# Kernel optimization log

Hardware: AMD Instinct MI355X
Metric: run time of the kernel (lower is better)

Reference implementation:

```python
import jax, jax.numpy as jnp
import numpy as np

NUM_LOCAL = 4      # num_local_experts
E_TOTAL = 8        # local + unpopular experts
HIDDEN = 1024
FFN = 4 * HIDDEN
CAP = 2048         # tokens (capacity) per expert
D0 = 1             # leading dim of inputs / output_tensor


def setup_inputs() -> dict:
    key = jax.random.key(0)
    k_in, k_w0, k_w3 = jax.random.split(key, 3)
    inputs = jax.random.normal(k_in, (D0, E_TOTAL, CAP, HIDDEN), dtype=jnp.float32)
    # gating-activity indicator per expert; all-ones -> all unpopular experts active
    output_tensor = jnp.ones((D0, E_TOTAL), dtype=jnp.float32)
    # stacked per-expert MLP weights (torch Linear convention: [out, in])
    w0 = jax.random.normal(k_w0, (E_TOTAL, FFN, HIDDEN), dtype=jnp.float32) * 0.02
    w3 = jax.random.normal(k_w3, (E_TOTAL, HIDDEN, FFN), dtype=jnp.float32) * 0.02
    return {"output_tensor": output_tensor, "inputs": inputs, "w0": w0, "w3": w3}


def reference(output_tensor, inputs, w0, w3):
    # Grouped 2-layer MLP per expert: x @ w0^T -> GELU -> @ w3^T
    # b: D0, e: expert, c: capacity, d: hidden, f: ffn
    h = jnp.einsum('becd,efd->becf', inputs, w0)
    h = jax.nn.gelu(h, approximate=False)  # torch nn.GELU default = exact erf
    out = jnp.einsum('becf,edf->becd', h, w3)
    # unpopular experts with zero activity produce zeros (scatter-into-zeros combine)
    unpop_mask = jnp.sum(output_tensor[:, NUM_LOCAL:], axis=0) != 0  # [E_unpop]
    full_mask = jnp.concatenate(
        [jnp.ones((NUM_LOCAL,), dtype=bool), unpop_mask])  # locals always computed
    out = out * full_mask[None, :, None, None].astype(out.dtype)
    return out
```

## Files before the change

### kernel.cpp

```cpp
#include <hip/hip_runtime.h>
#include <math.h>

#define E_TOTAL 8
#define NUM_LOCAL 4
#define HIDDEN 1024
#define FFN 4096
#define CAP 2048

typedef unsigned short ushort_t;
typedef __attribute__((ext_vector_type(8))) short short8;
typedef __attribute__((ext_vector_type(8))) unsigned short u16x8;
typedef __attribute__((ext_vector_type(4))) float f32x4;

__device__ __forceinline__ unsigned short f2bf(float f) {
  unsigned int u = __float_as_uint(f);
  u += 0x7FFFu + ((u >> 16) & 1u);
  return (unsigned short)(u >> 16);
}

__device__ __forceinline__ void gload_lds16(const void* g, void* l) {
  __builtin_amdgcn_global_load_lds(
      (const __attribute__((address_space(1))) void*)g,
      (__attribute__((address_space(3))) void*)l,
      16, 0, 0);
}

__global__ __launch_bounds__(256) void cvt_kernel(const float4* __restrict__ s,
                                                  u16x8* __restrict__ d) {
  const size_t i = (size_t)blockIdx.x * 256 + threadIdx.x;
  float4 a = s[2 * i], b = s[2 * i + 1];
  u16x8 o;
  o[0] = f2bf(a.x); o[1] = f2bf(a.y); o[2] = f2bf(a.z); o[3] = f2bf(a.w);
  o[4] = f2bf(b.x); o[5] = f2bf(b.y); o[6] = f2bf(b.z); o[7] = f2bf(b.w);
  d[i] = o;
}

template <int M, int N, int K, bool GELU_OUT>
__global__ __launch_bounds__(256, 2) void gemm_nt(
    const ushort_t* __restrict__ A, const ushort_t* __restrict__ B,
    void* __restrict__ Cout, const float* __restrict__ ot, int d0) {
  __shared__ ushort_t lds_a[128 * 64];
  __shared__ ushort_t lds_b[128 * 64];

  const int e = blockIdx.z;
  const int bm = blockIdx.x * 128;
  const int bn = blockIdx.y * 128;
  const int t = threadIdx.x;
  const int wave = t >> 6, lane = t & 63;
  const int wr = wave >> 1, wc = wave & 1;
  const int quad = lane >> 4, l16 = lane & 15;
  const int r8 = lane >> 3;
  const int s8 = lane & 7;
  const int g8 = (s8 + r8) & 7;

  const ushort_t* Ag = A + (size_t)e * M * K + (size_t)(bm + r8) * K + g8 * 8;
  const ushort_t* Bg = B + (size_t)e * N * K + (size_t)(bn + r8) * K + g8 * 8;

  f32x4 acc[4][4];
#pragma unroll
  for (int i = 0; i < 4; ++i)
#pragma unroll
    for (int j = 0; j < 4; ++j) {
      f32x4 z = {0.f, 0.f, 0.f, 0.f};
      acc[i][j] = z;
    }

  for (int kb = 0; kb < K / 64; ++kb) {
    const size_t ko = (size_t)kb * 64;
#pragma unroll
    for (int j = 0; j < 4; ++j) {
      const int R = (j * 4 + wave) * 8;
      gload_lds16(Ag + ko + (size_t)R * K, &lds_a[R * 64]);
      gload_lds16(Bg + ko + (size_t)R * K, &lds_b[R * 64]);
    }
    __syncthreads();

#pragma unroll
    for (int ks = 0; ks < 2; ++ks) {
      short8 af[4], bfr[4];
      const int c = ks * 4 + quad;
#pragma unroll
      for (int i = 0; i < 4; ++i) {
        const int ra = wr * 64 + i * 16 + l16;
        const int rb = wc * 64 + i * 16 + l16;
        af[i]  = *(const short8*)&lds_a[ra * 64 + ((c - ra) & 7) * 8];
        bfr[i] = *(const short8*)&lds_b[rb * 64 + ((c - rb) & 7) * 8];
      }
#pragma unroll
      for (int mi = 0; mi < 4; ++mi)
#pragma unroll
        for (int ni = 0; ni < 4; ++ni)
          acc[mi][ni] = __builtin_amdgcn_mfma_f32_16x16x32_bf16(
              af[mi], bfr[ni], acc[mi][ni], 0, 0, 0);
    }
    __syncthreads();
  }

  if (GELU_OUT) {
    ushort_t* C = (ushort_t*)Cout + (size_t)e * M * N +
                  (size_t)(bm + wr * 64) * N + (bn + wc * 64);
#pragma unroll
    for (int mi = 0; mi < 4; ++mi)
#pragma unroll
      for (int r = 0; r < 4; ++r) {
        const int row = mi * 16 + quad * 4 + r;
#pragma unroll
        for (int ni = 0; ni < 4; ++ni) {
          float v = acc[mi][ni][r];
          v = 0.5f * v * (1.f + erff(v * 0.70710678118654752f));
          C[(size_t)row * N + ni * 16 + l16] = f2bf(v);
        }
      }
  } else {
    float mask = 1.f;
    if (e >= NUM_LOCAL) {
      float s = 0.f;
      for (int b = 0; b < d0; ++b) s += ot[b * E_TOTAL + e];
      mask = (s != 0.f) ? 1.f : 0.f;
    }
    float* C = (float*)Cout + (size_t)e * M * N +
               (size_t)(bm + wr * 64) * N + (bn + wc * 64);
#pragma unroll
    for (int mi = 0; mi < 4; ++mi)
#pragma unroll
      for (int r = 0; r < 4; ++r) {
        const int row = mi * 16 + quad * 4 + r;
#pragma unroll
        for (int ni = 0; ni < 4; ++ni)
          C[(size_t)row * N + ni * 16 + l16] = acc[mi][ni][r] * mask;
      }
  }
}

extern "C" void kernel_launch(void* const* d_in, const int* in_sizes, int n_in,
                              void* d_out, int out_size, void* d_ws,
                              size_t ws_size, hipStream_t stream) {
  const float* ot = (const float*)d_in[0];
  const float* x  = (const float*)d_in[1];
  const float* w0 = (const float*)d_in[2];
  const float* w3 = (const float*)d_in[3];
  const int d0 = in_sizes[0] / E_TOTAL;

  char* ws = (char*)d_ws;
  ushort_t* xb  = (ushort_t*)ws;
  ushort_t* w0b = (ushort_t*)(ws + (size_t)32 * 1024 * 1024);
  ushort_t* w3b = (ushort_t*)ws;
  ushort_t* h   = (ushort_t*)(ws + (size_t)96 * 1024 * 1024);

  const int nx = E_TOTAL * CAP * HIDDEN;
  const int nw = E_TOTAL * FFN * HIDDEN;

  cvt_kernel<<<nx / (256 * 8), 256, 0, stream>>>((const float4*)x, (u16x8*)xb);
  cvt_kernel<<<nw / (256 * 8), 256, 0, stream>>>((const float4*)w0, (u16x8*)w0b);

  gemm_nt<CAP, FFN, HIDDEN, true>
      <<<dim3(CAP / 128, FFN / 128, E_TOTAL), 256, 0, stream>>>(
          xb, w0b, h, nullptr, d0);

  cvt_kernel<<<nw / (256 * 8), 256, 0, stream>>>((const float4*)w3, (u16x8*)w3b);

  gemm_nt<CAP, HIDDEN, FFN, false>
      <<<dim3(CAP / 128, HIDDEN / 128, E_TOTAL), 256, 0, stream>>>(
          h, w3b, d_out, ot, d0);
}
```

Baseline: 674.3 us.

## Rewrite grouped GEMM as 256x256 8-wave double-buffered pipelined kernel with fast GELU

```diff
diff --git a/kernel.cpp b/kernel.cpp
--- a/kernel.cpp
+++ b/kernel.cpp
@@ -23,6 +23,19 @@
       (const __attribute__((address_space(1))) void*)g,
       (__attribute__((address_space(3))) void*)l,
       16, 0, 0);
+}
+
+__device__ __forceinline__ float fast_gelu(float v) {
+  const float x = v * 0.70710678118654752f;
+  const float ax = fabsf(x);
+  const float t = 1.f / (1.f + 0.3275911f * ax);
+  const float p =
+      t * (0.254829592f +
+           t * (-0.284496736f +
+                t * (1.421413741f + t * (-1.453152027f + t * 1.061405429f))));
+  float erfv = 1.f - p * __expf(-ax * ax);
+  erfv = copysignf(erfv, x);
+  return 0.5f * v * (1.f + erfv);
 }
 
 __global__ __launch_bounds__(256) void cvt_kernel(const float4* __restrict__ s,
@@ -35,81 +48,146 @@
   d[i] = o;
 }
 
+template <int KD>
+__device__ __forceinline__ void stage_half(const ushort_t* g, char* dst,
+                                           int tid) {
+  gload_lds16(g, dst + tid * 16);
+  gload_lds16(g + (size_t)64 * KD, dst + 8192 + tid * 16);
+}
+
+#define LOAD_A4(F0)                                                          \
+  do {                                                                       \
+    _Pragma("unroll") for (int ks = 0; ks < 2; ++ks)                         \
+    _Pragma("unroll") for (int i = 0; i < 4; ++i)                            \
+      af[i][ks] = *(const short8*)(sAc + aoff[ks] + ((F0) + i) * 2048);      \
+  } while (0)
+
+#define LOAD_B2(J0)                                                          \
+  do {                                                                       \
+    _Pragma("unroll") for (int ks = 0; ks < 2; ++ks)                         \
+    _Pragma("unroll") for (int j = 0; j < 2; ++j)                            \
+      bf[(J0) + j][ks] =                                                     \
+          *(const short8*)(sBc + boff[ks] + ((J0) + j) * 2048);              \
+  } while (0)
+
+#define MFMA16(MI0, NJ0)                                                     \
+  do {                                                                       \
+    __builtin_amdgcn_s_setprio(1);                                           \
+    _Pragma("unroll") for (int ks = 0; ks < 2; ++ks)                         \
+    _Pragma("unroll") for (int i = 0; i < 4; ++i)                            \
+    _Pragma("unroll") for (int j = 0; j < 2; ++j)                            \
+      acc[(MI0) + i][(NJ0) + j] = __builtin_amdgcn_mfma_f32_16x16x32_bf16(   \
+          af[i][ks], bf[(NJ0) + j][ks], acc[(MI0) + i][(NJ0) + j], 0, 0, 0); \
+    __builtin_amdgcn_s_setprio(0);                                           \
+  } while (0)
+
+#define PHASE_SYNC()                                                         \
+  __builtin_amdgcn_s_barrier();                                              \
+  asm volatile("s_waitcnt lgkmcnt(0)" ::: "memory");                         \
+  __builtin_amdgcn_sched_barrier(0)
+
 template <int M, int N, int K, bool GELU_OUT>
-__global__ __launch_bounds__(256, 2) void gemm_nt(
+__global__ __launch_bounds__(512, 2) void gemm_nt8(
     const ushort_t* __restrict__ A, const ushort_t* __restrict__ B,
     void* __restrict__ Cout, const float* __restrict__ ot, int d0) {
-  __shared__ ushort_t lds_a[128 * 64];
-  __shared__ ushort_t lds_b[128 * 64];
+  __shared__ char sA[2][32768];
+  __shared__ char sB[2][32768];
+  constexpr int NT = K / 64;
+  static_assert(NT >= 2, "pipeline needs >=2 K-tiles");
 
   const int e = blockIdx.z;
-  const int bm = blockIdx.x * 128;
-  const int bn = blockIdx.y * 128;
-  const int t = threadIdx.x;
-  const int wave = t >> 6, lane = t & 63;
-  const int wr = wave >> 1, wc = wave & 1;
+  const int bm = blockIdx.x * 256;
+  const int bn = blockIdx.y * 256;
+  const int tid = threadIdx.x;
+  const int lane = tid & 63, wv = tid >> 6;
+  const int wr = wv >> 2, wc = wv & 3;
   const int quad = lane >> 4, l16 = lane & 15;
-  const int r8 = lane >> 3;
-  const int s8 = lane & 7;
-  const int g8 = (s8 + r8) & 7;
-
-  const ushort_t* Ag = A + (size_t)e * M * K + (size_t)(bm + r8) * K + g8 * 8;
-  const ushort_t* Bg = B + (size_t)e * N * K + (size_t)(bn + r8) * K + g8 * 8;
-
-  f32x4 acc[4][4];
-#pragma unroll
-  for (int i = 0; i < 4; ++i)
+  const int swz = l16 & 7;
+
+  const int rp = tid >> 3;
+  const int cs = (tid & 7) ^ (rp & 7);
+  const ushort_t* gA = A + (size_t)e * M * K + (size_t)(bm + rp) * K + cs * 8;
+  const ushort_t* gB = B + (size_t)e * N * K + (size_t)(bn + rp) * K + cs * 8;
+
+  int aoff[2], boff[2];
+#pragma unroll
+  for (int ks = 0; ks < 2; ++ks) {
+    aoff[ks] = (wr * 128 + l16) * 128 + (((ks * 4 + quad) ^ swz) << 4);
+    boff[ks] = (wc * 64 + l16) * 128 + (((ks * 4 + quad) ^ swz) << 4);
+  }
+
+  f32x4 acc[8][4];
+#pragma unroll
+  for (int i = 0; i < 8; ++i)
 #pragma unroll
     for (int j = 0; j < 4; ++j) {
       f32x4 z = {0.f, 0.f, 0.f, 0.f};
       acc[i][j] = z;
     }
 
-  for (int kb = 0; kb < K / 64; ++kb) {
-    const size_t ko = (size_t)kb * 64;
-#pragma unroll
-    for (int j = 0; j < 4; ++j) {
-      const int R = (j * 4 + wave) * 8;
-      gload_lds16(Ag + ko + (size_t)R * K, &lds_a[R * 64]);
-      gload_lds16(Bg + ko + (size_t)R * K, &lds_b[R * 64]);
+  short8 af[4][2];
+  short8 bf[4][2];
+
+  stage_half<K>(gA, sA[0], tid);
+  stage_half<K>(gA + (size_t)128 * K, sA[0] + 16384, tid);
+  stage_half<K>(gB, sB[0], tid);
+  stage_half<K>(gB + (size_t)128 * K, sB[0] + 16384, tid);
+  stage_half<K>(gB + 64, sB[1], tid);
+  stage_half<K>(gB + (size_t)128 * K + 64, sB[1] + 16384, tid);
+  asm volatile("s_waitcnt vmcnt(4)" ::: "memory");
+  __builtin_amdgcn_sched_barrier(0);
+  __builtin_amdgcn_s_barrier();
+
+#pragma unroll 2
+  for (int t = 0; t < NT; ++t) {
+    char* sAc = sA[t & 1];
+    char* sBc = sB[t & 1];
+    char* sAn = sA[(t + 1) & 1];
+    const size_t ko1 = (size_t)(t + 1) * 64;
+    const size_t ko2 = (size_t)(t + 2) * 64;
+
+    LOAD_A4(0);
+    LOAD_B2(0);
+    if (t + 1 < NT) stage_half<K>(gA + ko1, sAn, tid);
+    PHASE_SYNC();
+    MFMA16(0, 0);
+    __builtin_amdgcn_s_barrier();
+
+    LOAD_B2(2);
+    if (t + 1 < NT) stage_half<K>(gA + (size_t)128 * K + ko1, sAn + 16384, tid);
+    PHASE_SYNC();
+    MFMA16(0, 2);
+    __builtin_amdgcn_s_barrier();
+
+    LOAD_A4(4);
+    if (t + 2 < NT) stage_half<K>(gB + ko2, sBc, tid);
+    PHASE_SYNC();
+    MFMA16(4, 0);
+    __builtin_amdgcn_s_barrier();
+
+    if (t + 2 < NT) stage_half<K>(gB + (size_t)128 * K + ko2, sBc + 16384, tid);
+    PHASE_SYNC();
+    MFMA16(4, 2);
+    if (t + 2 < NT) {
+      asm volatile("s_waitcnt vmcnt(4)" ::: "memory");
+    } else {
+      asm volatile("s_waitcnt vmcnt(0)" ::: "memory");
     }
-    __syncthreads();
-
-#pragma unroll
-    for (int ks = 0; ks < 2; ++ks) {
-      short8 af[4], bfr[4];
-      const int c = ks * 4 + quad;
-#pragma unroll
-      for (int i = 0; i < 4; ++i) {
-        const int ra = wr * 64 + i * 16 + l16;
-        const int rb = wc * 64 + i * 16 + l16;
-        af[i]  = *(const short8*)&lds_a[ra * 64 + ((c - ra) & 7) * 8];
-        bfr[i] = *(const short8*)&lds_b[rb * 64 + ((c - rb) & 7) * 8];
-      }
-#pragma unroll
-      for (int mi = 0; mi < 4; ++mi)
-#pragma unroll
-        for (int ni = 0; ni < 4; ++ni)
-          acc[mi][ni] = __builtin_amdgcn_mfma_f32_16x16x32_bf16(
-              af[mi], bfr[ni], acc[mi][ni], 0, 0, 0);
-    }
-    __syncthreads();
+    __builtin_amdgcn_sched_barrier(0);
+    __builtin_amdgcn_s_barrier();
   }
 
   if (GELU_OUT) {
     ushort_t* C = (ushort_t*)Cout + (size_t)e * M * N +
-                  (size_t)(bm + wr * 64) * N + (bn + wc * 64);
-#pragma unroll
-    for (int mi = 0; mi < 4; ++mi)
+                  (size_t)(bm + wr * 128) * N + (bn + wc * 64);
+#pragma unroll
+    for (int mi = 0; mi < 8; ++mi)
 #pragma unroll
       for (int r = 0; r < 4; ++r) {
         const int row = mi * 16 + quad * 4 + r;
 #pragma unroll
-        for (int ni = 0; ni < 4; ++ni) {
-          float v = acc[mi][ni][r];
-          v = 0.5f * v * (1.f + erff(v * 0.70710678118654752f));
-          C[(size_t)row * N + ni * 16 + l16] = f2bf(v);
-        }
+        for (int ni = 0; ni < 4; ++ni)
+          C[(size_t)row * N + ni * 16 + l16] = f2bf(fast_gelu(acc[mi][ni][r]));
       }
   } else {
     float mask = 1.f;
@@ -119,9 +197,9 @@
       mask = (s != 0.f) ? 1.f : 0.f;
     }
     float* C = (float*)Cout + (size_t)e * M * N +
-               (size_t)(bm + wr * 64) * N + (bn + wc * 64);
-#pragma unroll
-    for (int mi = 0; mi < 4; ++mi)
+               (size_t)(bm + wr * 128) * N + (bn + wc * 64);
+#pragma unroll
+    for (int mi = 0; mi < 8; ++mi)
 #pragma unroll
       for (int r = 0; r < 4; ++r) {
         const int row = mi * 16 + quad * 4 + r;
@@ -153,13 +231,13 @@
   cvt_kernel<<<nx / (256 * 8), 256, 0, stream>>>((const float4*)x, (u16x8*)xb);
   cvt_kernel<<<nw / (256 * 8), 256, 0, stream>>>((const float4*)w0, (u16x8*)w0b);
 
-  gemm_nt<CAP, FFN, HIDDEN, true>
-      <<<dim3(CAP / 128, FFN / 128, E_TOTAL), 256, 0, stream>>>(
+  gemm_nt8<CAP, FFN, HIDDEN, true>
+      <<<dim3(CAP / 256, FFN / 256, E_TOTAL), 512, 0, stream>>>(
           xb, w0b, h, nullptr, d0);
 
   cvt_kernel<<<nw / (256 * 8), 256, 0, stream>>>((const float4*)w3, (u16x8*)w3b);
 
-  gemm_nt<CAP, HIDDEN, FFN, false>
-      <<<dim3(CAP / 128, HIDDEN / 128, E_TOTAL), 256, 0, stream>>>(
+  gemm_nt8<CAP, HIDDEN, FFN, false>
+      <<<dim3(CAP / 256, HIDDEN / 256, E_TOTAL), 512, 0, stream>>>(
           h, w3b, d_out, ot, d0);
 }
```

After: 646.8 us. 1.04x faster.
